# Kernel optimization log

Hardware: AMD Instinct MI355X
Metric: run time of the kernel (lower is better)

## Reference

```python
import jax, jax.numpy as jnp
from jax import lax
import numpy as np

# dims
B, L, M = 16, 512, 32
PRED, P, S, D = 96, 16, 8, 128
NST, DC, EXP, NL = 16, 4, 2, 4
N = (L - P) // S + 1          # 63 patches
DI = EXP * D                  # 256 d_inner
DTR = (D + 15) // 16          # 8 dt_rank


def setup_inputs() -> dict:
    key = jax.random.key(0)
    ks = jax.random.split(key, 16)
    r = lambda i, shape, s=0.02: jax.random.normal(ks[i], shape, dtype=jnp.float32) * s
    return {
        "x": jax.random.normal(ks[0], (B, L, M), dtype=jnp.float32),
        "patch_w": r(1, (D, P), 0.1), "patch_b": jnp.zeros((D,), jnp.float32),
        "pos_embed": r(2, (1, N, D)),
        "alpha": jnp.ones((NL, NL), jnp.float32), "beta": jnp.ones((NL, NL), jnp.float32),
        "theta": jnp.ones((NL, NL + 1), jnp.float32), "gamma": jnp.ones((NL, NL), jnp.float32),
        "tok_norm_w": jnp.ones((NL, D), jnp.float32), "tok_norm_b": jnp.zeros((NL, D), jnp.float32),
        "ch_norm_w": jnp.ones((NL, D), jnp.float32), "ch_norm_b": jnp.zeros((NL, D), jnp.float32),
        # 3 Mamba roles per layer: 0=token, 1=channel-fwd, 2=channel-bwd
        "in_proj_w": r(3, (NL, 3, 2 * DI, D), 0.05),
        "conv_w": r(4, (NL, 3, DI, DC), 0.1), "conv_b": jnp.zeros((NL, 3, DI), jnp.float32),
        "x_proj_w": r(5, (NL, 3, DTR + 2 * NST, DI), 0.05),
        "dt_proj_w": r(6, (NL, 3, DI, DTR), 0.1), "dt_proj_b": r(7, (NL, 3, DI), 0.5),
        "A_log": jnp.broadcast_to(jnp.log(jnp.arange(1, NST + 1, dtype=jnp.float32)), (NL, 3, DI, NST)) + 0.0,
        "D_ssm": jnp.ones((NL, 3, DI), jnp.float32),
        "out_proj_w": r(8, (NL, 3, D, DI), 0.05),
        "n2d_w1": jnp.ones((D,), jnp.float32), "n2d_b1": jnp.zeros((D,), jnp.float32),
        "n2d_w2": jnp.ones((N,), jnp.float32), "n2d_b2": jnp.zeros((N,), jnp.float32),
        "head_w": r(9, (PRED, N * D), 0.01), "head_b": jnp.zeros((PRED,), jnp.float32),
    }


def _ln(x, w, b):
    mu = x.mean(-1, keepdims=True)
    var = x.var(-1, keepdims=True)
    return (x - mu) * lax.rsqrt(var + 1e-5) * w + b


def _mamba(x, in_w, cw, cb, xw, dtw, dtb, a_log, dp, out_w):
    """Standard Mamba block. x: (b, s, D) -> (b, s, D)."""
    bsz = x.shape[0]
    xz = x @ in_w.T                                   # (b,s,2*DI)
    xi, z = jnp.split(xz, 2, axis=-1)
    # causal depthwise conv over seq
    xt = jnp.pad(xi.transpose(0, 2, 1), ((0, 0), (0, 0), (DC - 1, 0)))
    conv = lax.conv_general_dilated(xt, cw[:, None, :], (1,), 'VALID',
                                    dimension_numbers=('NCH', 'OIH', 'NCH'),
                                    feature_group_count=DI)
    u = jax.nn.silu(conv + cb[None, :, None]).transpose(0, 2, 1)  # (b,s,DI)
    xdbl = u @ xw.T
    dt, Bm, Cm = jnp.split(xdbl, [DTR, DTR + NST], axis=-1)
    dt = jax.nn.softplus(dt @ dtw.T + dtb)            # (b,s,DI)
    A = -jnp.exp(a_log)                               # (DI,NST)

    def step(h, inp):
        dt_t, b_t, c_t, u_t = inp                     # (b,DI),(b,NST),(b,NST),(b,DI)
        h = h * jnp.exp(dt_t[:, :, None] * A) + (dt_t * u_t)[:, :, None] * b_t[:, None, :]
        return h, jnp.einsum('bdn,bn->bd', h, c_t)

    h0 = jnp.zeros((bsz, DI, NST), x.dtype)
    _, ys = lax.scan(step, h0, (dt.swapaxes(0, 1), Bm.swapaxes(0, 1),
                                Cm.swapaxes(0, 1), u.swapaxes(0, 1)))
    y = ys.swapaxes(0, 1) + u * dp                    # D skip
    y = y * jax.nn.silu(z)
    return y @ out_w.T


def reference(x, patch_w, patch_b, pos_embed, alpha, beta, theta, gamma,
              tok_norm_w, tok_norm_b, ch_norm_w, ch_norm_b,
              in_proj_w, conv_w, conv_b, x_proj_w, dt_proj_w, dt_proj_b,
              A_log, D_ssm, out_proj_w, n2d_w1, n2d_b1, n2d_w2, n2d_b2,
              head_w, head_b):
    means = x.mean(1, keepdims=True)
    stds = jnp.std(x, axis=1, keepdims=True, ddof=1) + 1e-5   # torch unbiased std
    xn = ((x - means) / stds).transpose(0, 2, 1)              # (B,M,L)
    idx = jnp.arange(N)[:, None] * S + jnp.arange(P)[None, :]
    patches = xn[:, :, idx].reshape(B * M, N, P)              # unfold
    h = patches @ patch_w.T + patch_b + pos_embed             # (B*M,N,D)

    def mp(l, r):
        return (in_proj_w[l, r], conv_w[l, r], conv_b[l, r], x_proj_w[l, r],
                dt_proj_w[l, r], dt_proj_b[l, r], A_log[l, r], D_ssm[l, r], out_proj_w[l, r])

    yT, yC = [h], [h]
    for l in range(NL):
        a = jax.nn.softmax(alpha[l, :l + 1])
        bb = jax.nn.softmax(beta[l, :l + 1])
        tok_in = sum(a[i] * yT[i] + bb[i] * yC[i] for i in range(l + 1))
        tok = _mamba(_ln(tok_in, tok_norm_w[l], tok_norm_b[l]), *mp(l, 0)) + tok_in
        yT.append(tok)

        t = jax.nn.softmax(theta[l, :l + 2])
        g = jax.nn.softmax(gamma[l, :l + 1])
        ch_in = sum(t[i] * yT[i] for i in range(l + 2)) + sum(g[i] * yC[i] for i in range(l + 1))
        chr_ = ch_in.reshape(B, M, N, D).transpose(0, 2, 1, 3).reshape(B * N, M, D)
        chr_ = _ln(chr_, ch_norm_w[l], ch_norm_b[l])
        fwd = _mamba(chr_, *mp(l, 1))
        bwd = jnp.flip(_mamba(jnp.flip(chr_, 1), *mp(l, 2)), 1)
        ch_out = (fwd + bwd).reshape(B, N, M, D).transpose(0, 2, 1, 3).reshape(B * M, N, D) + ch_in
        yC.append(ch_out)

    out = yC[-1]
    out = _ln(out, n2d_w1, n2d_b1)                            # Norm2D
    out = _ln(out.swapaxes(-1, -2), n2d_w2, n2d_b2).swapaxes(-1, -2)
    out = out.reshape(B * M, N * D) @ head_w.T + head_b
    out = out.reshape(B, M, PRED).transpose(0, 2, 1)          # (B,PRED,M)
    return out * stds + means
```

## Files before the change

kernel.cpp:

```cpp
#include <hip/hip_runtime.h>
#include <hip/hip_bf16.h>
#include <cstddef>

#define Bq    16
#define Lq    512
#define Mq    32
#define PREDq 96
#define Pq    16
#define Sq    8
#define Dq    128
#define NSTq  16
#define DCq   4
#define NLq   4
#define Nq    63
#define DIq   256
#define DTRq  8
#define TOKq  32256
#define BMq   512
#define BNq   1008

typedef __attribute__((ext_vector_type(8))) short short8;
typedef __attribute__((ext_vector_type(4))) float f32x4;
typedef __attribute__((ext_vector_type(2))) float f32x2;
typedef __hip_bfloat16 bf16;

constexpr size_t HSZB      = (size_t)TOKq * Dq;
constexpr size_t OFF_MEANS = 0;
constexpr size_t OFF_STDS  = 512;
constexpr size_t OFF_PART  = 50176;
constexpr size_t OFF_HISTB = 640000;
constexpr size_t OFF_MIX   = OFF_HISTB + 9 * (HSZB / 2);
constexpr size_t OFF_XD    = OFF_MIX + (size_t)TOKq * 128;
constexpr size_t OFF_XZ2   = OFF_XD + (size_t)TOKq * 80;
constexpr size_t OFF_UC    = OFF_XZ2 + (size_t)TOKq * 512;
constexpr size_t OFF_LNB   = OFF_UC + (size_t)TOKq * 256;
constexpr size_t OFF_WB    = OFF_LNB + (size_t)TOKq * 64;
constexpr size_t WS_FLOATS = OFF_WB + 1038336;
constexpr size_t WBE_IN   = 0;
constexpr size_t WBE_X    = 786432;
constexpr size_t WBE_OUT  = 909312;
constexpr size_t WBE_HEAD = 1302528;
constexpr int    WB_TOTAL = 2076672;

__device__ __forceinline__ float silu_f(float v) { return v / (1.f + __expf(-v)); }

__device__ __forceinline__ f32x2 bfup2(const bf16* p) {
    unsigned int v = *(const unsigned int*)p;
    f32x2 r;
    r.x = __uint_as_float(v << 16);
    r.y = __uint_as_float(v & 0xffff0000u);
    return r;
}
__device__ __forceinline__ void bfpack2(float f0, float f1, bf16* dst) {
    bf16 b0 = __float2bfloat16(f0), b1 = __float2bfloat16(f1);
    unsigned int u = (unsigned int)*(unsigned short*)&b0 |
                     ((unsigned int)*(unsigned short*)&b1 << 16);
    *(unsigned int*)dst = u;
}

__global__ __launch_bounds__(256) void f2b_all(const float* __restrict__ w_in,
                                               const float* __restrict__ w_x,
                                               const float* __restrict__ w_out,
                                               const float* __restrict__ w_head,
                                               bf16* __restrict__ d) {
    int i = blockIdx.x * 256 + threadIdx.x;
    if (i >= WB_TOTAL) return;
    float v;
    if (i < 786432)        v = w_in[i];
    else if (i < 909312)   v = w_x[i - 786432];
    else if (i < 1302528)  v = w_out[i - 909312];
    else                   v = w_head[i - 1302528];
    d[i] = __float2bfloat16(v);
}

__global__ __launch_bounds__(256) void stats_kernel(const float* __restrict__ x,
                                                    float* __restrict__ means,
                                                    float* __restrict__ stds) {
    int bm = blockIdx.x; int b = bm >> 5, m = bm & 31;
    int tid = threadIdx.x;
    float s = 0.f, ss = 0.f;
    for (int l = tid; l < Lq; l += 256) {
        float v = x[((size_t)b * Lq + l) * Mq + m];
        s += v; ss += v * v;
    }
#pragma unroll
    for (int o = 32; o >= 1; o >>= 1) { s += __shfl_xor(s, o); ss += __shfl_xor(ss, o); }
    __shared__ float sh0[4], sh1[4];
    if ((tid & 63) == 0) { sh0[tid >> 6] = s; sh1[tid >> 6] = ss; }
    __syncthreads();
    if (tid == 0) {
        float S  = sh0[0] + sh0[1] + sh0[2] + sh0[3];
        float SS = sh1[0] + sh1[1] + sh1[2] + sh1[3];
        float mean = S * (1.f / (float)Lq);
        float var  = (SS - (float)Lq * mean * mean) * (1.f / (float)(Lq - 1));
        means[bm] = mean;
        stds[bm]  = sqrtf(fmaxf(var, 0.f)) + 1e-5f;
    }
}

__global__ __launch_bounds__(128) void patch_embed(const float* __restrict__ x,
                                                   const float* __restrict__ means,
                                                   const float* __restrict__ stds,
                                                   const float* __restrict__ pw,
                                                   const float* __restrict__ pb,
                                                   const float* __restrict__ pos,
                                                   bf16* __restrict__ h) {
    int blk = blockIdx.x;
    int bm = blk / Nq, n = blk - bm * Nq;
    int b = bm >> 5, m = bm & 31;
    int d = threadIdx.x;
    __shared__ float sx[Pq];
    if (d < Pq) {
        int l = n * Sq + d;
        sx[d] = (x[((size_t)b * Lq + l) * Mq + m] - means[bm]) / stds[bm];
    }
    __syncthreads();
    float acc = pb[d];
#pragma unroll
    for (int p = 0; p < Pq; p++) acc += sx[p] * pw[d * Pq + p];
    h[(size_t)blk * Dq + d] = __float2bfloat16(acc + pos[n * Dq + d]);
}

template<int CONVM, int KSKIP, int NT, int MR = 128>
__global__ __launch_bounds__(256) void gemm_k(
        const bf16* __restrict__ A, int lda,
        const bf16* __restrict__ Bw, const bf16* __restrict__ Bw2, int ldb,
        const float* __restrict__ resid, int ldr,
        float* __restrict__ C, bf16* __restrict__ Cb, int ldc,
        int M, int N, int Klen, int kstride, size_t csplit,
        int accum, int rowmap,
        int slen, const float* __restrict__ cw, const float* __restrict__ cb,
        int Mhalf, int ahalfcol, int choff, int gsilu,
        bf16* __restrict__ ucout) {
    constexpr int WR = MR / 4;
    constexpr int MS = WR / 16;
    __shared__ __align__(16) short Al[MR * 40];
    __shared__ __align__(16) short Bl[NT * 40];
    int tid = threadIdx.x;
    int wave = tid >> 6, lane = tid & 63;
    int m0 = blockIdx.y * MR, n0 = blockIdx.x * NT;
    int kbase = blockIdx.z * kstride;
    constexpr int NS = NT / 16;
    f32x4 acc[MS][NS];
#pragma unroll
    for (int i = 0; i < MS; i++)
#pragma unroll
        for (int j = 0; j < NS; j++) acc[i][j] = (f32x4){0.f, 0.f, 0.f, 0.f};

    int mlane = lane & 15, koff = (lane >> 4) * 8;
    const uint4 Z4 = {0u, 0u, 0u, 0u};

    {
        int ar = tid >> 1, ah = tid & 1;
        int brr = (NT == 128) ? (tid >> 1) : (tid >> 2);
        int bqh = (NT == 128) ? (tid & 1) : (tid & 3);
        uint4 av0, av1, bv0, bv1;
        av0 = av1 = bv0 = bv1 = Z4;
        auto loadAB = [&](int kk0) {
            int gcol = kk0 + ah * 16;
            if (KSKIP && kk0 >= 256) gcol += 256;
            const bf16* asrc = A + (size_t)(m0 + ar) * lda + gcol;
            av0 = *(const uint4*)asrc;
            av1 = *(const uint4*)(asrc + 8);
            const bf16* bb = Bw;
            if (NT == 128) {
                int bc = kk0 + bqh * 16;
                if (KSKIP && kk0 >= 256) { bb = Bw2; bc -= 256; }
                int gn = n0 + brr;
                if (gn < N) {
                    const bf16* bsrc = bb + (size_t)gn * ldb + bc;
                    bv0 = *(const uint4*)bsrc;
                    bv1 = *(const uint4*)(bsrc + 8);
                } else { bv0 = Z4; bv1 = Z4; }
            } else {
                int bc = kk0 + bqh * 8;
                if (KSKIP && kk0 >= 256) { bb = Bw2; bc -= 256; }
                int gn = n0 + brr;
                bv0 = (gn < N) ? *(const uint4*)(bb + (size_t)gn * ldb + bc) : Z4;
            }
        };
        loadAB(kbase);
        for (int k0 = 0; k0 < Klen; k0 += 32) {
            *(uint4*)&Al[ar * 40 + ah * 16]     = av0;
            *(uint4*)&Al[ar * 40 + ah * 16 + 8] = av1;
            if (NT == 128) {
                *(uint4*)&Bl[brr * 40 + bqh * 16]     = bv0;
                *(uint4*)&Bl[brr * 40 + bqh * 16 + 8] = bv1;
            } else {
                *(uint4*)&Bl[brr * 40 + bqh * 8] = bv0;
            }
            __syncthreads();
            if (k0 + 32 < Klen) loadAB(kbase + k0 + 32);
            short8 afr[MS];
#pragma unroll
            for (int ms = 0; ms < MS; ms++)
                afr[ms] = *(const short8*)&Al[(wave * WR + ms * 16 + mlane) * 40 + koff];
#pragma unroll
            for (int ns = 0; ns < NS; ns++) {
                short8 bfr = *(const short8*)&Bl[(ns * 16 + mlane) * 40 + koff];
#pragma unroll
                for (int ms = 0; ms < MS; ms++)
                    acc[ms][ns] = __builtin_amdgcn_mfma_f32_16x16x32_bf16(afr[ms], bfr, acc[ms][ns], 0, 0, 0);
            }
            __syncthreads();
        }
    }

    float* Cz = C + (size_t)blockIdx.z * csplit;
#pragma unroll
    for (int ms = 0; ms < MS; ms++) {
#pragma unroll
        for (int ns = 0; ns < NS; ns++) {
            int n = n0 + ns * 16 + mlane;
            if (n >= N) continue;
#pragma unroll
            for (int r = 0; r < 4; r++) {
                int m = m0 + wave * WR + ms * 16 + (lane >> 4) * 4 + r;
                int orow = m, ocol = n;
                if (rowmap) {
                    int bn = m >> 5, mm = m & 31;
                    int b = bn / Nq, nn = bn - b * Nq;
                    orow = (b * Mq + mm) * Nq + nn;
                }
                float v = acc[ms][ns][r];
                if (resid) v += resid[(size_t)orow * ldr + ocol];
                if (Cb) {
                    if (gsilu && ((ocol >> 8) & 1)) v = silu_f(v);
                    Cb[(size_t)orow * ldc + ocol] = __float2bfloat16(v);
                } else {
                    size_t o = (size_t)orow * ldc + ocol;
                    if (accum) Cz[o] += v; else Cz[o] = v;
                }
            }
        }
    }
}

template<int KSKIP, int ROWMAP, int MIXMODE>
__global__ __launch_bounds__(256) void gemm_mix(
        const bf16* __restrict__ A,
        const bf16* __restrict__ Bw, const bf16* __restrict__ Bw2,
        const float* __restrict__ resid,
        bf16* __restrict__ hb, int hwrite, int l,
        const float* __restrict__ mw0, const float* __restrict__ mw1,
        const float* __restrict__ lnw, const float* __restrict__ lnb,
        float* __restrict__ mixout, bf16* __restrict__ lnbout) {
    constexpr int KLEN = KSKIP ? 512 : 256;
    __shared__ __align__(16) short Al[64 * 40];
    __shared__ __align__(16) short Bl[128 * 40];
    int tid = threadIdx.x;
    int wave = tid >> 6, lane = tid & 63;
    int mlane = lane & 15, koff = (lane >> 4) * 8;
    int m0 = blockIdx.x * 64;

    f32x4 acc[8];
#pragma unroll
    for (int j = 0; j < 8; j++) acc[j] = (f32x4){0.f, 0.f, 0.f, 0.f};

    int ar = tid >> 2, ah = tid & 3;
    int br = tid >> 1, bq = tid & 1;
    uint4 av, bv0, bv1;
    auto loadAB = [&](int kk0) {
        int gcol = kk0 + ah * 8;
        if (KSKIP && kk0 >= 256) gcol += 256;
        av = *(const uint4*)(A + (size_t)(m0 + ar) * 1024 + gcol);
        const bf16* bb = Bw;
        int bc = kk0 + bq * 16;
        if (KSKIP && kk0 >= 256) { bb = Bw2; bc -= 256; }
        const bf16* bsrc = bb + (size_t)br * 256 + bc;
        bv0 = *(const uint4*)bsrc;
        bv1 = *(const uint4*)(bsrc + 8);
    };
    loadAB(0);
    for (int k0 = 0; k0 < KLEN; k0 += 32) {
        *(uint4*)&Al[ar * 40 + ah * 8]      = av;
        *(uint4*)&Bl[br * 40 + bq * 16]     = bv0;
        *(uint4*)&Bl[br * 40 + bq * 16 + 8] = bv1;
        __syncthreads();
        if (k0 + 32 < KLEN) loadAB(k0 + 32);
        short8 a = *(const short8*)&Al[(wave * 16 + mlane) * 40 + koff];
#pragma unroll
        for (int ns = 0; ns < 8; ns++) {
            short8 b = *(const short8*)&Bl[(ns * 16 + mlane) * 40 + koff];
            acc[ns] = __builtin_amdgcn_mfma_f32_16x16x32_bf16(a, b, acc[ns], 0, 0, 0);
        }
        __syncthreads();
    }

    float w0[5], w1[4];
    int ct = 0, cg = 0;
    if (MIXMODE == 0) {
        ct = l + 2; cg = l + 1;
        float m0v = -1e30f, m1v = -1e30f;
        for (int i = 0; i < ct; i++) { w0[i] = mw0[l * 5 + i]; m0v = fmaxf(m0v, w0[i]); }
        for (int i = 0; i < cg; i++) { w1[i] = mw1[l * 4 + i]; m1v = fmaxf(m1v, w1[i]); }
        float s0 = 0.f, s1 = 0.f;
        for (int i = 0; i < ct; i++) { w0[i] = __expf(w0[i] - m0v); s0 += w0[i]; }
        for (int i = 0; i < cg; i++) { w1[i] = __expf(w1[i] - m1v); s1 += w1[i]; }
        float i0 = 1.f / s0, i1 = 1.f / s1;
        for (int i = 0; i < ct; i++) w0[i] *= i0;
        for (int i = 0; i < cg; i++) w1[i] *= i1;
    } else if (MIXMODE == 1) {
        int lt = l + 1;
        ct = lt + 1; cg = lt + 1;
        float m0v = -1e30f, m1v = -1e30f;
        for (int i = 0; i < ct; i++) {
            w0[i] = mw0[lt * 4 + i]; w1[i] = mw1[lt * 4 + i];
            m0v = fmaxf(m0v, w0[i]); m1v = fmaxf(m1v, w1[i]);
        }
        float s0 = 0.f, s1 = 0.f;
        for (int i = 0; i < ct; i++) {
            w0[i] = __expf(w0[i] - m0v); s0 += w0[i];
            w1[i] = __expf(w1[i] - m1v); s1 += w1[i];
        }
        float i0 = 1.f / s0, i1 = 1.f / s1;
        for (int i = 0; i < ct; i++) { w0[i] *= i0; w1[i] *= i1; }
    }

#pragma unroll
    for (int r = 0; r < 4; r++) {
        int m = m0 + wave * 16 + (lane >> 4) * 4 + r;
        int orow = m;
        if (ROWMAP) {
            int bn = m >> 5, mm = m & 31;
            int b = bn / Nq, nn = bn - b * Nq;
            orow = (b * Mq + mm) * Nq + nn;
        }
        size_t t128 = (size_t)orow * 128;
        float hv[8];
#pragma unroll
        for (int ns = 0; ns < 8; ns++) {
            int col = ns * 16 + mlane;
            float v = acc[ns][r] + resid[t128 + col];
            bf16 hvb = __float2bfloat16(v);
            hb[(size_t)hwrite * HSZB + t128 + col] = hvb;
            hv[ns] = __bfloat162float(hvb);
        }
        float mixv[8];
        if (MIXMODE == 2) {
#pragma unroll
            for (int ns = 0; ns < 8; ns++) mixv[ns] = hv[ns];
        } else if (MIXMODE == 0) {
#pragma unroll
            for (int ns = 0; ns < 8; ns++) mixv[ns] = 0.f;
            for (int i = 0; i < ct; i++) {
                int bi = (i == 0) ? 0 : i;
                if (bi == hwrite) {
#pragma unroll
                    for (int ns = 0; ns < 8; ns++) mixv[ns] += w0[i] * hv[ns];
                } else {
                    const bf16* yp = hb + (size_t)bi * HSZB + t128;
#pragma unroll
                    for (int ns = 0; ns < 8; ns++)
                        mixv[ns] += w0[i] * __bfloat162float(yp[ns * 16 + mlane]);
                }
            }
            for (int i = 0; i < cg; i++) {
                int bi = (i == 0) ? 0 : 4 + i;
                const bf16* yp = hb + (size_t)bi * HSZB + t128;
#pragma unroll
                for (int ns = 0; ns < 8; ns++)
                    mixv[ns] += w1[i] * __bfloat162float(yp[ns * 16 + mlane]);
            }
        } else {
#pragma unroll
            for (int ns = 0; ns < 8; ns++) mixv[ns] = 0.f;
            for (int i = 0; i < ct; i++) {
                int bt = (i == 0) ? 0 : i;
                int bc = (i == 0) ? 0 : 4 + i;
                const bf16* ytp = hb + (size_t)bt * HSZB + t128;
                if (bc == hwrite) {
#pragma unroll
                    for (int ns = 0; ns < 8; ns++)
                        mixv[ns] += w0[i] * __bfloat162float(ytp[ns * 16 + mlane]) + w1[i] * hv[ns];
                } else {
                    const bf16* ycp = hb + (size_t)bc * HSZB + t128;
#pragma unroll
                    for (int ns = 0; ns < 8; ns++)
                        mixv[ns] += w0[i] * __bfloat162float(ytp[ns * 16 + mlane]) +
                                    w1[i] * __bfloat162float(ycp[ns * 16 + mlane]);
                }
            }
        }
        float s = 0.f, ss = 0.f;
#pragma unroll
        for (int ns = 0; ns < 8; ns++) { s += mixv[ns]; ss += mixv[ns] * mixv[ns]; }
#pragma unroll
        for (int o = 8; o >= 1; o >>= 1) { s += __shfl_xor(s, o); ss += __shfl_xor(ss, o); }
        float mean = s * (1.f / 128.f);
        float var  = ss * (1.f / 128.f) - mean * mean;
        float rstd = rsqrtf(var + 1e-5f);
        if (MIXMODE == 2) {
#pragma unroll
            for (int ns = 0; ns < 8; ns++) {
                int col = ns * 16 + mlane;
                mixout[t128 + col] = (mixv[ns] - mean) * rstd * lnw[col] + lnb[col];
            }
        } else {
#pragma unroll
            for (int ns = 0; ns < 8; ns++) mixout[t128 + ns * 16 + mlane] = mixv[ns];
            size_t lbase;
            if (MIXMODE == 0) {
                int bm = orow / Nq, nn = orow - bm * Nq, b = bm >> 5, mq = bm & 31;
                lbase = (size_t)((b * Nq + nn) * Mq + mq) * 128;
            } else {
                lbase = t128;
            }
#pragma unroll
            for (int ns = 0; ns < 8; ns++) {
                int col = ns * 16 + mlane;
                lnbout[lbase + col] =
                    __float2bfloat16((mixv[ns] - mean) * rstd * lnw[col] + lnb[col]);
            }
        }
    }
}

template<int SLEN, int ROWS>
__global__ __launch_bounds__(256) void scan_f(bf16* __restrict__ xz2,
                                              const float* __restrict__ dtw,
                                              const float* __restrict__ dtb,
                                              const float* __restrict__ alog,
                                              const float* __restrict__ Dp,
                                              const float* __restrict__ cw,
                                              const float* __restrict__ cb,
                                              const bf16* __restrict__ xw,
                                              const bf16* __restrict__ xw2,
                                              int nb, int dual) {
    constexpr int UST = 264;
    __shared__ __align__(16) bf16 u_l[ROWS * UST];
    __shared__ __align__(16) float qlds[SLEN * 40];
    int bid = blockIdx.x;
    int half = (dual && bid >= nb) ? 1 : 0;
    int row = bid - half * nb;
    int rev = half;
    int tid = threadIdx.x;
    int d = tid;
    int wave = tid >> 6, lane = tid & 63;
    int mlane = lane & 15, koff = (lane >> 4) * 8;

    size_t xbase = (size_t)row * SLEN * 1024 + (size_t)half * 512 + d;
    size_t base  = xbase;

    float ucur[8], zcur[8];
#pragma unroll
    for (int i = 0; i < 8; i++) {
        int s = rev ? (SLEN - 1 - i) : i;
        zcur[i] = __bfloat162float(xz2[base + (size_t)s * 1024 + 256]);
    }
    const float* al = alog + half * 4096 + d * 16;
    float a0 = -__expf(al[0]);
    bool fast = true;
#pragma unroll
    for (int j = 1; j < 16; j++) {
        float aj = -__expf(al[j]);
        fast = fast && (fabsf(aj - a0 * (float)(j + 1)) < 1e-5f * (float)(j + 1));
    }
    f32x2 dw2[4];
#pragma unroll
    for (int r = 0; r < 4; r++)
        dw2[r] = (f32x2){dtw[half * 2048 + d * 8 + 2 * r], dtw[half * 2048 + d * 8 + 2 * r + 1]};
    float dbv = dtb[half * 256 + d], Dv = Dp[half * 256 + d];

    {
        float c0 = cw[half * 1024 + d * 4 + 0];
        float c1 = cw[half * 1024 + d * 4 + 1];
        float c2 = cw[half * 1024 + d * 4 + 2];
        float c3 = cw[half * 1024 + d * 4 + 3];
        float cbv = cb[half * 256 + d];
        constexpr int NCC = (SLEN + 7) / 8;
        float xc[8], xn[8];
#pragma unroll
        for (int i = 0; i < 8; i++) {
            int st = i < SLEN ? i : SLEN - 1;
            int s = rev ? (SLEN - 1 - st) : st;
            xc[i] = __bfloat162float(xz2[xbase + (size_t)s * 1024]);
        }
        float g1 = 0.f, g2 = 0.f, g3 = 0.f;
        for (int c = 0; c < NCC; c++) {
            if (c + 1 < NCC) {
#pragma unroll
                for (int i = 0; i < 8; i++) {
                    int st = (c + 1) * 8 + i; st = st < SLEN ? st : SLEN - 1;
                    int s = rev ? (SLEN - 1 - st) : st;
                    xn[i] = __bfloat162float(xz2[xbase + (size_t)s * 1024]);
                }
            }
#pragma unroll
            for (int i = 0; i < 8; i++) {
                int st = c * 8 + i;
                if (st < SLEN) {
                    int s = rev ? (SLEN - 1 - st) : st;
                    float cur = xc[i];
                    float ac = cbv;
                    if (st >= 3) ac += c0 * g3;
                    if (st >= 2) ac += c1 * g2;
                    if (st >= 1) ac += c2 * g1;
                    ac += c3 * cur;
                    bf16 ub = __float2bfloat16(silu_f(ac));
                    u_l[s * UST + d] = ub;
                    if (c == 0) ucur[i] = __bfloat162float(ub);
                    g3 = g2; g2 = g1; g1 = cur;
                }
            }
#pragma unroll
            for (int i = 0; i < 8; i++) xc[i] = xn[i];
        }
        for (int s = SLEN; s < ROWS; s++) u_l[s * UST + d] = __float2bfloat16(0.f);
    }
    __syncthreads();

    {
        const bf16* xwp = half ? xw2 : xw;
        constexpr int RT = ROWS / 16;
        constexpr int NTILES = RT * 3;
        const short8 bz = {0, 0, 0, 0, 0, 0, 0, 0};
        for (int tI = wave; tI < NTILES; tI += 4) {
            int tr = tI / 3, tc = tI - tr * 3;
            int gn = tc * 16 + mlane;
            bool okn = gn < 40;
            f32x4 acc = (f32x4){0.f, 0.f, 0.f, 0.f};
#pragma unroll
            for (int kk = 0; kk < 256; kk += 32) {
                short8 a = *(const short8*)&u_l[(tr * 16 + mlane) * UST + kk + koff];
                short8 b = okn ? *(const short8*)(xwp + (size_t)gn * 256 + kk + koff) : bz;
                acc = __builtin_amdgcn_mfma_f32_16x16x32_bf16(a, b, acc, 0, 0, 0);
            }
#pragma unroll
            for (int r = 0; r < 4; r++) {
                int s = tr * 16 + (lane >> 4) * 4 + r;
                if (okn && s < SLEN) qlds[s * 40 + gn] = acc[r];
            }
        }
    }

    f32x2 h2[8];
#pragma unroll
    for (int j = 0; j < 8; j++) h2[j] = (f32x2){0.f, 0.f};
    constexpr int NCH = (SLEN + 7) / 8;
    __syncthreads();

    float unxt[8], znxt[8];
    for (int c = 0; c < NCH; c++) {
        if (c + 1 < NCH) {
#pragma unroll
            for (int i = 0; i < 8; i++) {
                int st = (c + 1) * 8 + i; st = st < SLEN ? st : SLEN - 1;
                int s = rev ? (SLEN - 1 - st) : st;
                unxt[i] = __bfloat162float(u_l[s * UST + d]);
                znxt[i] = __bfloat162float(xz2[base + (size_t)s * 1024 + 256]);
            }
        }
#pragma unroll
        for (int i = 0; i < 8; i++) {
            int st = c * 8 + i;
            if (st < SLEN) {
                int s = rev ? (SLEN - 1 - st) : st;
                const float4* qv = (const float4*)&qlds[s * 40];
                float4 qa = qv[0], qb = qv[1];
                float uc_v = ucur[i];
                f32x2 acc2 = dw2[0] * (f32x2){qa.x, qa.y};
                acc2 += dw2[1] * (f32x2){qa.z, qa.w};
                acc2 += dw2[2] * (f32x2){qb.x, qb.y};
                acc2 += dw2[3] * (f32x2){qb.z, qb.w};
                float dtv = dbv + acc2.x + acc2.y;
                dtv = fmaxf(dtv, 0.f) + __logf(1.f + __expf(-fabsf(dtv)));
                float du = dtv * uc_v;
                float y;
                if (fast) {
                    float p1 = __expf(dtv * a0);
                    float p2 = p1 * p1;
                    f32x2 pp = (f32x2){p2, p2};
                    f32x2 e2[8];
                    e2[0] = (f32x2){p1, p2};
#pragma unroll
                    for (int j = 1; j < 8; j++) e2[j] = e2[j - 1] * pp;
                    f32x2 du2 = (f32x2){du, du};
                    f32x2 y2 = (f32x2){0.f, 0.f};
                    float4 B0 = qv[2], B1 = qv[3], B2 = qv[4], B3 = qv[5];
                    float4 C0 = qv[6], C1 = qv[7], C2 = qv[8], C3 = qv[9];
                    f32x2 bb[8] = {{B0.x, B0.y}, {B0.z, B0.w}, {B1.x, B1.y}, {B1.z, B1.w},
                                   {B2.x, B2.y}, {B2.z, B2.w}, {B3.x, B3.y}, {B3.z, B3.w}};
                    f32x2 cc[8] = {{C0.x, C0.y}, {C0.z, C0.w}, {C1.x, C1.y}, {C1.z, C1.w},
                                   {C2.x, C2.y}, {C2.z, C2.w}, {C3.x, C3.y}, {C3.z, C3.w}};
#pragma unroll
                    for (int j = 0; j < 8; j++) {
                        h2[j] = h2[j] * e2[j] + du2 * bb[j];
                        y2 += h2[j] * cc[j];
                    }
                    y = y2.x + y2.y;
                } else {
                    const float* q = &qlds[s * 40];
                    y = 0.f;
#pragma unroll
                    for (int j = 0; j < 16; j++) {
                        float e = __expf(dtv * (-__expf(al[j])));
                        float hh = h2[j >> 1][j & 1];
                        hh = hh * e + du * q[8 + j];
                        h2[j >> 1][j & 1] = hh;
                        y += hh * q[24 + j];
                    }
                }
                xz2[base + (size_t)s * 1024] =
                    __float2bfloat16((y + uc_v * Dv) * zcur[i]);
            }
        }
#pragma unroll
        for (int i = 0; i < 8; i++) { ucur[i] = unxt[i]; zcur[i] = znxt[i]; }
    }
}

__global__ __launch_bounds__(256) void mix_ln_tok(const bf16* __restrict__ hb,
                                                 float* __restrict__ mixb, bf16* __restrict__ lnb_out,
                                                 const float* __restrict__ alpha,
                                                 const float* __restrict__ beta,
                                                 const float* __restrict__ lnw,
                                                 const float* __restrict__ lnb, int l) {
    int t = blockIdx.x * 4 + (threadIdx.x >> 6), d = threadIdx.x & 63;
    int cnt = l + 1;
    float aw[4], bw[4];
    float amax = -1e30f, bmax = -1e30f;
    for (int i = 0; i < cnt; i++) {
        aw[i] = alpha[l * 4 + i]; bw[i] = beta[l * 4 + i];
        amax = fmaxf(amax, aw[i]); bmax = fmaxf(bmax, bw[i]);
    }
    float as = 0.f, bs = 0.f;
    for (int i = 0; i < cnt; i++) {
        aw[i] = __expf(aw[i] - amax); as += aw[i];
        bw[i] = __expf(bw[i] - bmax); bs += bw[i];
    }
    float ai = 1.f / as, bi = 1.f / bs;
    float v0 = 0.f, v1 = 0.f;
    for (int i = 0; i < cnt; i++) {
        const bf16* yt = hb + (size_t)(i == 0 ? 0 : i) * HSZB + (size_t)t * 128 + 2 * d;
        const bf16* yc = hb + (size_t)(i == 0 ? 0 : 4 + i) * HSZB + (size_t)t * 128 + 2 * d;
        f32x2 vt = bfup2(yt), vc = bfup2(yc);
        float wa = aw[i] * ai, wb = bw[i] * bi;
        v0 += wa * vt.x + wb * vc.x;
        v1 += wa * vt.y + wb * vc.y;
    }
    *(f32x2*)&mixb[(size_t)t * 128 + 2 * d] = (f32x2){v0, v1};
    float s = v0 + v1, ss = v0 * v0 + v1 * v1;
#pragma unroll
    for (int o = 32; o >= 1; o >>= 1) { s += __shfl_xor(s, o); ss += __shfl_xor(ss, o); }
    float mean = s * (1.f / 128.f);
    float var  = ss * (1.f / 128.f) - mean * mean;
    float rstd = rsqrtf(var + 1e-5f);
    f32x2 w2 = *(const f32x2*)&lnw[2 * d];
    f32x2 b2 = *(const f32x2*)&lnb[2 * d];
    bfpack2((v0 - mean) * rstd * w2.x + b2.x,
            (v1 - mean) * rstd * w2.y + b2.y,
            lnb_out + (size_t)t * 128 + 2 * d);
}

__global__ __launch_bounds__(256) void final_ln2(const float* __restrict__ in,
                                                 const float* __restrict__ w2,
                                                 const float* __restrict__ b2,
                                                 bf16* __restrict__ out) {
    int idx = blockIdx.x * 256 + threadIdx.x;
    if (idx >= BMq * Dq) return;
    int bm = idx >> 7, d = idx & 127;
    float s = 0.f, ss = 0.f;
    for (int n = 0; n < Nq; n++) {
        float v = in[((size_t)bm * Nq + n) * 128 + d];
        s += v; ss += v * v;
    }
    float mean = s * (1.f / (float)Nq);
    float var  = ss * (1.f / (float)Nq) - mean * mean;
    float rstd = rsqrtf(var + 1e-5f);
    for (int n = 0; n < Nq; n++) {
        float v = in[((size_t)bm * Nq + n) * 128 + d];
        out[((size_t)bm * Nq + n) * 128 + d] = __float2bfloat16((v - mean) * rstd * w2[n] + b2[n]);
    }
}

__global__ __launch_bounds__(256) void finalize_kernel(const float* __restrict__ part,
                                                       const float* __restrict__ bias,
                                                       const float* __restrict__ means,
                                                       const float* __restrict__ stds,
                                                       float* __restrict__ out) {
    int idx = blockIdx.x * 256 + threadIdx.x;
    if (idx >= Bq * PREDq * Mq) return;
    int b = idx / (PREDq * Mq);
    int r = idx - b * PREDq * Mq;
    int pr = r >> 5, m = r & 31;
    int bm = b * Mq + m;
    float s = bias[pr];
#pragma unroll
    for (int z = 0; z < 12; z++) s += part[(size_t)z * BMq * PREDq + (size_t)bm * PREDq + pr];
    out[idx] = s * stds[bm] + means[bm];
}

extern "C" void kernel_launch(void* const* d_in, const int* in_sizes, int n_in,
                              void* d_out, int out_size, void* d_ws, size_t ws_size,
                              hipStream_t stream) {
    if (ws_size < WS_FLOATS * sizeof(float)) return;

    const float* x          = (const float*)d_in[0];
    const float* patch_w    = (const float*)d_in[1];
    const float* patch_b    = (const float*)d_in[2];
    const float* pos_embed  = (const float*)d_in[3];
    const float* alpha      = (const float*)d_in[4];
    const float* beta       = (const float*)d_in[5];
    const float* theta      = (const float*)d_in[6];
    const float* gamma      = (const float*)d_in[7];
    const float* tok_norm_w = (const float*)d_in[8];
    const float* tok_norm_b = (const float*)d_in[9];
    const float* ch_norm_w  = (const float*)d_in[10];
    const float* ch_norm_b  = (const float*)d_in[11];
    const float* in_proj_w  = (const float*)d_in[12];
    const float* conv_w     = (const float*)d_in[13];
    const float* conv_b     = (const float*)d_in[14];
    const float* x_proj_w   = (const float*)d_in[15];
    const float* dt_proj_w  = (const float*)d_in[16];
    const float* dt_proj_b  = (const float*)d_in[17];
    const float* A_log      = (const float*)d_in[18];
    const float* D_ssm      = (const float*)d_in[19];
    const float* out_proj_w = (const float*)d_in[20];
    const float* n2d_w1     = (const float*)d_in[21];
    const float* n2d_b1     = (const float*)d_in[22];
    const float* n2d_w2     = (const float*)d_in[23];
    const float* n2d_b2     = (const float*)d_in[24];
    const float* head_w     = (const float*)d_in[25];
    const float* head_b     = (const float*)d_in[26];

    float* W   = (float*)d_ws;
    float* out = (float*)d_out;
    bf16* WB   = (bf16*)(W + OFF_WB);
    bf16* HB   = (bf16*)(W + OFF_HISTB);
    bf16* LNB  = (bf16*)(W + OFF_LNB);
    bf16* XZ2  = (bf16*)(W + OFF_XZ2);
    float* MIX = W + OFF_MIX;

    f2b_all<<<(WB_TOTAL + 255) / 256, 256, 0, stream>>>(
        in_proj_w, x_proj_w, out_proj_w, head_w, WB);

    stats_kernel<<<BMq, 256, 0, stream>>>(x, W + OFF_MEANS, W + OFF_STDS);
    patch_embed<<<TOKq, 128, 0, stream>>>(x, W + OFF_MEANS, W + OFF_STDS,
                                          patch_w, patch_b, pos_embed, HB);

    mix_ln_tok<<<TOKq / 4, 256, 0, stream>>>(HB, MIX, LNB, alpha, beta,
                                             tok_norm_w, tok_norm_b, 0);

    for (int l = 0; l < NLq; l++) {
        size_t o0 = (size_t)(l * 3 + 0), o1 = (size_t)(l * 3 + 1), o2 = (size_t)(l * 3 + 2);

        gemm_k<0, 0, 128><<<dim3(4, 252, 1), 256, 0, stream>>>(
            LNB, 128, WB + WBE_IN + o0 * 65536, nullptr, 128, nullptr, 0,
            nullptr, XZ2, 1024, TOKq, 512, 128, 0, 0, 0, 0,
            0, nullptr, nullptr, 0, 0, 0, 1, nullptr);
        scan_f<Nq, 64><<<BMq, 256, 0, stream>>>(
            XZ2, dt_proj_w + o0 * 2048, dt_proj_b + o0 * 256,
            A_log + o0 * 4096, D_ssm + o0 * 256,
            conv_w + o0 * 1024, conv_b + o0 * 256,
            WB + WBE_X + o0 * 10240, nullptr, BMq, 0);
        gemm_mix<0, 0, 0><<<504, 256, 0, stream>>>(
            XZ2, WB + WBE_OUT + o0 * 32768, nullptr, MIX,
            HB, 1 + l, l, theta, gamma,
            ch_norm_w + l * Dq, ch_norm_b + l * Dq, MIX, LNB);

        gemm_k<0, 0, 128><<<dim3(8, 252, 1), 256, 0, stream>>>(
            LNB, 128, WB + WBE_IN + o1 * 65536, nullptr, 128, nullptr, 0,
            nullptr, XZ2, 1024, TOKq, 1024, 128, 0, 0, 0, 0,
            0, nullptr, nullptr, 0, 0, 0, 1, nullptr);
        scan_f<Mq, 32><<<2 * BNq, 256, 0, stream>>>(
            XZ2, dt_proj_w + o1 * 2048, dt_proj_b + o1 * 256,
            A_log + o1 * 4096, D_ssm + o1 * 256,
            conv_w + o1 * 1024, conv_b + o1 * 256,
            WB + WBE_X + o1 * 10240, WB + WBE_X + o2 * 10240, BNq, 1);
        if (l < NLq - 1) {
            gemm_mix<1, 1, 1><<<504, 256, 0, stream>>>(
                XZ2, WB + WBE_OUT + o1 * 32768, WB + WBE_OUT + o2 * 32768, MIX,
                HB, 5 + l, l, alpha, beta,
                tok_norm_w + (l + 1) * Dq, tok_norm_b + (l + 1) * Dq, MIX, LNB);
        } else {
            gemm_mix<1, 1, 2><<<504, 256, 0, stream>>>(
                XZ2, WB + WBE_OUT + o1 * 32768, WB + WBE_OUT + o2 * 32768, MIX,
                HB, 5 + l, l, nullptr, nullptr,
                n2d_w1, n2d_b1, MIX, nullptr);
        }
    }

    final_ln2<<<(BMq * Dq + 255) / 256, 256, 0, stream>>>(MIX, n2d_w2, n2d_b2, LNB);
    gemm_k<0, 0, 64><<<dim3(2, 4, 12), 256, 0, stream>>>(
        LNB, Nq * Dq, WB + WBE_HEAD, nullptr, Nq * Dq, nullptr, 0,
        W + OFF_PART, nullptr, PREDq, BMq, PREDq, 672, 672,
        (size_t)BMq * PREDq, 0, 0, 0, nullptr, nullptr, 0, 0, 0, 0, nullptr);
    finalize_kernel<<<(Bq * PREDq * Mq + 255) / 256, 256, 0, stream>>>(
        W + OFF_PART, head_b, W + OFF_MEANS, W + OFF_STDS, out);
}
```

Measured before the change: 1.028 ms.

## Fuse next Mamba in_proj GEMM into gemm_mix epilogue via shared LN tile

The gemm_mix kernel now keeps the LayerNormed 64x128 tile in shared memory and immediately runs the following in_proj GEMM (4 or 8 column chunks of 128) against it. The result goes straight to XZ2 with the silu gate applied and the row remap. This removes the separate in_proj gemm_k launches inside the layer loop and the LNB write/read round trip. The cost is extra LDS, longer per-block work in gemm_mix with only 504 blocks, and a possible write-after-read hazard on XZ2, which is read as A and written as output in the same kernel.

```diff
diff --git a/kernel.cpp b/kernel.cpp
--- a/kernel.cpp
+++ b/kernel.cpp
@@ -236,7 +236,7 @@
     }
 }
 
-template<int KSKIP, int ROWMAP, int MIXMODE>
+template<int KSKIP, int ROWMAP, int MIXMODE, int INPROJ>
 __global__ __launch_bounds__(256) void gemm_mix(
         const bf16* __restrict__ A,
         const bf16* __restrict__ Bw, const bf16* __restrict__ Bw2,
@@ -244,10 +244,12 @@
         bf16* __restrict__ hb, int hwrite, int l,
         const float* __restrict__ mw0, const float* __restrict__ mw1,
         const float* __restrict__ lnw, const float* __restrict__ lnb,
-        float* __restrict__ mixout, bf16* __restrict__ lnbout) {
+        float* __restrict__ mixout, bf16* __restrict__ lnbout,
+        const bf16* __restrict__ Wi, bf16* __restrict__ xzout) {
     constexpr int KLEN = KSKIP ? 512 : 256;
     __shared__ __align__(16) short Al[64 * 40];
     __shared__ __align__(16) short Bl[128 * 40];
+    __shared__ __align__(16) bf16 Aln[INPROJ ? 64 * 132 : 1];
     int tid = threadIdx.x;
     int wave = tid >> 6, lane = tid & 63;
     int mlane = lane & 15, koff = (lane >> 4) * 8;
@@ -409,8 +411,62 @@
 #pragma unroll
             for (int ns = 0; ns < 8; ns++) {
                 int col = ns * 16 + mlane;
-                lnbout[lbase + col] =
-                    __float2bfloat16((mixv[ns] - mean) * rstd * lnw[col] + lnb[col]);
+                bf16 lv = __float2bfloat16((mixv[ns] - mean) * rstd * lnw[col] + lnb[col]);
+                if (INPROJ) Aln[(m - m0) * 132 + col] = lv;
+                if (lnbout) lnbout[lbase + col] = lv;
+            }
+        }
+    }
+
+    if (INPROJ) {
+        int abr = tid >> 1, abq = tid & 1;
+        uint4 wv0, wv1;
+        auto loadW = [&](int it) {
+            int nc = it >> 2, kk = (it & 3) * 32;
+            const bf16* src = Wi + (size_t)(nc * 128 + abr) * 128 + kk + abq * 16;
+            wv0 = *(const uint4*)src;
+            wv1 = *(const uint4*)(src + 8);
+        };
+        loadW(0);
+        f32x4 acc2[8];
+        for (int it = 0; it < INPROJ * 4; it++) {
+            int nc = it >> 2, kk = (it & 3) * 32;
+            if ((it & 3) == 0) {
+#pragma unroll
+                for (int j = 0; j < 8; j++) acc2[j] = (f32x4){0.f, 0.f, 0.f, 0.f};
+            }
+            __syncthreads();
+            *(uint4*)&Bl[abr * 40 + abq * 16]     = wv0;
+            *(uint4*)&Bl[abr * 40 + abq * 16 + 8] = wv1;
+            __syncthreads();
+            if (it + 1 < INPROJ * 4) loadW(it + 1);
+            short8 a = *(const short8*)&Aln[(wave * 16 + mlane) * 132 + kk + koff];
+#pragma unroll
+            for (int ns = 0; ns < 8; ns++) {
+                short8 b = *(const short8*)&Bl[(ns * 16 + mlane) * 40 + koff];
+                acc2[ns] = __builtin_amdgcn_mfma_f32_16x16x32_bf16(a, b, acc2[ns], 0, 0, 0);
+            }
+            if ((it & 3) == 3) {
+#pragma unroll
+                for (int r = 0; r < 4; r++) {
+                    int m = m0 + wave * 16 + (lane >> 4) * 4 + r;
+                    int xrow;
+                    if (MIXMODE == 0) {
+                        int bm = m / Nq, nn = m - bm * Nq;
+                        xrow = ((bm >> 5) * Nq + nn) * Mq + (bm & 31);
+                    } else {
+                        int bn = m >> 5, mm = m & 31;
+                        int b = bn / Nq, nn = bn - b * Nq;
+                        xrow = (b * Mq + mm) * Nq + nn;
+                    }
+#pragma unroll
+                    for (int ns = 0; ns < 8; ns++) {
+                        int col = nc * 128 + ns * 16 + mlane;
+                        float v = acc2[ns][r];
+                        if ((col >> 8) & 1) v = silu_f(v);
+                        xzout[(size_t)xrow * 1024 + col] = __float2bfloat16(v);
+                    }
+                }
             }
         }
     }
@@ -741,43 +797,42 @@
 
     mix_ln_tok<<<TOKq / 4, 256, 0, stream>>>(HB, MIX, LNB, alpha, beta,
                                              tok_norm_w, tok_norm_b, 0);
+    gemm_k<0, 0, 128><<<dim3(4, 252, 1), 256, 0, stream>>>(
+        LNB, 128, WB + WBE_IN, nullptr, 128, nullptr, 0,
+        nullptr, XZ2, 1024, TOKq, 512, 128, 0, 0, 0, 0,
+        0, nullptr, nullptr, 0, 0, 0, 1, nullptr);
 
     for (int l = 0; l < NLq; l++) {
         size_t o0 = (size_t)(l * 3 + 0), o1 = (size_t)(l * 3 + 1), o2 = (size_t)(l * 3 + 2);
 
-        gemm_k<0, 0, 128><<<dim3(4, 252, 1), 256, 0, stream>>>(
-            LNB, 128, WB + WBE_IN + o0 * 65536, nullptr, 128, nullptr, 0,
-            nullptr, XZ2, 1024, TOKq, 512, 128, 0, 0, 0, 0,
-            0, nullptr, nullptr, 0, 0, 0, 1, nullptr);
         scan_f<Nq, 64><<<BMq, 256, 0, stream>>>(
             XZ2, dt_proj_w + o0 * 2048, dt_proj_b + o0 * 256,
             A_log + o0 * 4096, D_ssm + o0 * 256,
             conv_w + o0 * 1024, conv_b + o0 * 256,
             WB + WBE_X + o0 * 10240, nullptr, BMq, 0);
-        gemm_mix<0, 0, 0><<<504, 256, 0, stream>>>(
+        gemm_mix<0, 0, 0, 8><<<504, 256, 0, stream>>>(
             XZ2, WB + WBE_OUT + o0 * 32768, nullptr, MIX,
             HB, 1 + l, l, theta, gamma,
-            ch_norm_w + l * Dq, ch_norm_b + l * Dq, MIX, LNB);
-
-        gemm_k<0, 0, 128><<<dim3(8, 252, 1), 256, 0, stream>>>(
-            LNB, 128, WB + WBE_IN + o1 * 65536, nullptr, 128, nullptr, 0,
-            nullptr, XZ2, 1024, TOKq, 1024, 128, 0, 0, 0, 0,
-            0, nullptr, nullptr, 0, 0, 0, 1, nullptr);
+            ch_norm_w + l * Dq, ch_norm_b + l * Dq, MIX, nullptr,
+            WB + WBE_IN + o1 * 65536, XZ2);
+
         scan_f<Mq, 32><<<2 * BNq, 256, 0, stream>>>(
             XZ2, dt_proj_w + o1 * 2048, dt_proj_b + o1 * 256,
             A_log + o1 * 4096, D_ssm + o1 * 256,
             conv_w + o1 * 1024, conv_b + o1 * 256,
             WB + WBE_X + o1 * 10240, WB + WBE_X + o2 * 10240, BNq, 1);
         if (l < NLq - 1) {
-            gemm_mix<1, 1, 1><<<504, 256, 0, stream>>>(
+            gemm_mix<1, 1, 1, 4><<<504, 256, 0, stream>>>(
                 XZ2, WB + WBE_OUT + o1 * 32768, WB + WBE_OUT + o2 * 32768, MIX,
                 HB, 5 + l, l, alpha, beta,
-                tok_norm_w + (l + 1) * Dq, tok_norm_b + (l + 1) * Dq, MIX, LNB);
+                tok_norm_w + (l + 1) * Dq, tok_norm_b + (l + 1) * Dq, MIX, nullptr,
+                WB + WBE_IN + (size_t)((l + 1) * 3) * 65536, XZ2);
         } else {
-            gemm_mix<1, 1, 2><<<504, 256, 0, stream>>>(
+            gemm_mix<1, 1, 2, 0><<<504, 256, 0, stream>>>(
                 XZ2, WB + WBE_OUT + o1 * 32768, WB + WBE_OUT + o2 * 32768, MIX,
                 HB, 5 + l, l, nullptr, nullptr,
-                n2d_w1, n2d_b1, MIX, nullptr);
+                n2d_w1, n2d_b1, MIX, nullptr,
+                nullptr, nullptr);
         }
     }
 
```

Measured after the change: 1.296 ms. 1.26x slower.
